# Kernel optimization log

Hardware: AMD Instinct MI355X
Metric: run time of the kernel (lower is better)

The kernel has to match this reference:

```python
import jax, jax.numpy as jnp
import numpy as np

N = 262144  # nodes
E = 262144  # edges (child -> parent)
X = 128     # x_size
H = 128     # h_size


def setup_inputs() -> dict:
    key = jax.random.key(0)
    ks = jax.random.split(key, 10)
    s = 1.0 / np.sqrt(H)
    return {
        "token_embeds": jax.random.normal(ks[0], (N, X), jnp.float32),
        "h": jax.random.normal(ks[1], (N, H), jnp.float32),
        "c": jax.random.normal(ks[2], (N, H), jnp.float32),
        "src": jax.random.randint(ks[3], (E,), 0, N),
        "dst": jax.random.randint(ks[4], (E,), 0, N),
        "W_iou": jax.random.normal(ks[5], (3 * H, X), jnp.float32) * s,
        "U_iou": jax.random.normal(ks[6], (3 * H, H), jnp.float32) * s,
        "b_iou": jnp.zeros((1, 3 * H), jnp.float32),
        "U_f_w": jax.random.normal(ks[7], (H, H), jnp.float32) * s,
        "U_f_b": jnp.zeros((H,), jnp.float32),
        "W_f_w": jax.random.normal(ks[8], (H, X), jnp.float32) * s,
        "b_f": jnp.zeros((1, H), jnp.float32),
    }


def reference(token_embeds, h, c, src, dst, W_iou, U_iou, b_iou, U_f_w, U_f_b, W_f_w, b_f):
    # message + reduce: gather children's h/c and sum into parent mailboxes
    h_sum = jax.ops.segment_sum(h[src], dst, num_segments=N)  # [N,H]
    c_sum = jax.ops.segment_sum(c[src], dst, num_segments=N)  # [N,H]
    # forget gate is per-node, so sum_k f*c_k == f * sum_k c_k
    f = jax.nn.sigmoid(token_embeds @ W_f_w.T + h @ U_f_w.T + U_f_b + b_f)  # [N,H]
    c_red = f * c_sum
    iou = token_embeds @ W_iou.T + h_sum @ U_iou.T + b_iou  # [N,3H]
    i, o, u = jnp.split(iou, 3, axis=1)
    c_new = jax.nn.sigmoid(i) * jnp.tanh(u) + c_red
    h_new = jax.nn.sigmoid(o) * jnp.tanh(c_new)
    return h_new, c_new
```

## Files before the change

### kernel.cpp

```cpp
#include <hip/hip_runtime.h>
#include <hip/hip_bf16.h>
#include <cstdint>

#define HH 128
#define XX 128

typedef __attribute__((ext_vector_type(8))) short short8;
typedef __attribute__((ext_vector_type(4))) short short4_;
typedef __attribute__((ext_vector_type(4))) float float4_;
typedef __attribute__((ext_vector_type(8))) _Float16 half8_;

__device__ __forceinline__ float sigmoidf_(float x) {
  return 1.f / (1.f + __expf(-x));
}
__device__ __forceinline__ float tanhf_(float x) {
  float e = __expf(-2.f * fabsf(x));
  float t = (1.f - e) / (1.f + e);
  return copysignf(t, x);
}

__global__ __launch_bounds__(256) void hist_kernel(const int* __restrict__ dst,
                                                   int* __restrict__ cnt, int E) {
  int e = blockIdx.x * 256 + threadIdx.x;
  if (e < E) atomicAdd(&cnt[dst[e]], 1);
}

__global__ __launch_bounds__(256) void scan_block_sum(const int* __restrict__ cnt,
                                                      int* __restrict__ bsum) {
  __shared__ int red[256];
  int b = blockIdx.x, t = threadIdx.x;
  int base = b * 1024 + t * 4;
  int s = cnt[base] + cnt[base + 1] + cnt[base + 2] + cnt[base + 3];
  red[t] = s;
  __syncthreads();
  for (int off = 128; off > 0; off >>= 1) {
    if (t < off) red[t] += red[t + off];
    __syncthreads();
  }
  if (t == 0) bsum[b] = red[0];
}

__global__ __launch_bounds__(256) void scan_top(const int* __restrict__ bsum,
                                                int* __restrict__ boff,
                                                int* __restrict__ row_ptr, int N,
                                                int E) {
  __shared__ int tmp[256];
  int t = threadIdx.x;
  int own = bsum[t];
  tmp[t] = own;
  __syncthreads();
  for (int off = 1; off < 256; off <<= 1) {
    int x = (t >= off) ? tmp[t - off] : 0;
    __syncthreads();
    tmp[t] += x;
    __syncthreads();
  }
  boff[t] = tmp[t] - own;
  if (t == 0) row_ptr[N] = E;
}

__global__ __launch_bounds__(256) void scan_fill(const int* __restrict__ cnt,
                                                 const int* __restrict__ boff,
                                                 int* __restrict__ row_ptr,
                                                 int* __restrict__ row_fill) {
  __shared__ int tsum[256];
  int b = blockIdx.x, t = threadIdx.x;
  int base = b * 1024 + t * 4;
  int v0 = cnt[base], v1 = cnt[base + 1], v2 = cnt[base + 2], v3 = cnt[base + 3];
  int s = v0 + v1 + v2 + v3;
  tsum[t] = s;
  __syncthreads();
  for (int off = 1; off < 256; off <<= 1) {
    int x = (t >= off) ? tsum[t - off] : 0;
    __syncthreads();
    tsum[t] += x;
    __syncthreads();
  }
  int excl = tsum[t] - s + boff[b];
  int p0 = excl, p1 = p0 + v0, p2 = p1 + v1, p3 = p2 + v2;
  row_ptr[base] = p0;
  row_ptr[base + 1] = p1;
  row_ptr[base + 2] = p2;
  row_ptr[base + 3] = p3;
  row_fill[base] = p0;
  row_fill[base + 1] = p1;
  row_fill[base + 2] = p2;
  row_fill[base + 3] = p3;
}

__global__ __launch_bounds__(256) void fill_kernel(const int* __restrict__ src,
                                                   const int* __restrict__ dst,
                                                   int* __restrict__ row_fill,
                                                   int* __restrict__ edge_src,
                                                   int E) {
  int e = blockIdx.x * 256 + threadIdx.x;
  if (e >= E) return;
  int pos = atomicAdd(&row_fill[dst[e]], 1);
  edge_src[pos] = src[e];
}

__global__ __launch_bounds__(256) void prep_kernel(
    const float* __restrict__ W_iou, const float* __restrict__ U_iou,
    const float* __restrict__ b_iou, const float* __restrict__ U_f_w,
    const float* __restrict__ U_f_b, const float* __restrict__ W_f_w,
    const float* __restrict__ b_f, unsigned short* __restrict__ Bh,
    float* __restrict__ bias) {
  int tid = blockIdx.x * 256 + threadIdx.x;
  int kg = tid & 3;
  int c16 = (tid >> 2) & 15;
  int ks = (tid >> 6) & 7;
  int w = (tid >> 9) & 7;
  int g = (tid >> 12) & 3;
  int col = w * 16 + c16;
  int kbase = ks * 32 + kg * 8;
#pragma unroll
  for (int j = 0; j < 8; ++j) {
    int k = kbase + j;
    float v;
    if (g < 3) {
      v = (k < 128) ? W_iou[(size_t)(g * 128 + col) * 128 + k]
                    : U_iou[(size_t)(g * 128 + col) * 128 + (k - 128)];
    } else {
      v = (k < 128) ? W_f_w[(size_t)col * 128 + k]
                    : U_f_w[(size_t)col * 128 + (k - 128)];
    }
    Bh[(size_t)tid * 8 + j] = __builtin_bit_cast(unsigned short, (_Float16)v);
  }
  if (tid < 512) {
    int gg = tid >> 7, cc = tid & 127;
    bias[tid] = (gg < 3) ? b_iou[gg * 128 + cc] : (U_f_b[cc] + b_f[cc]);
  }
}


__device__ __forceinline__ void stage_f16(unsigned short* su, int a, int node,
                                          int k4, float4_ v) {
  unsigned short hq[4];
#pragma unroll
  for (int j = 0; j < 4; ++j)
    hq[j] = __builtin_bit_cast(unsigned short, (_Float16)v[j]);
  int off = k4 ^ ((node & 7) << 3);
  *reinterpret_cast<short4_*>(&su[a * 4096 + node * 128 + off]) =
      *reinterpret_cast<const short4_*>(hq);
}

__device__ __forceinline__ half8_ read_frag(const unsigned short* su, int a,
                                            int node, int kbase, int lane) {
  int k = kbase + ((lane >> 4) << 3);
  int off = k ^ ((node & 7) << 3);
  short8 s = *reinterpret_cast<const short8*>(&su[a * 4096 + node * 128 + off]);
  return __builtin_bit_cast(half8_, s);
}

__device__ __forceinline__ int cw(int row, int col) {
  return row * 128 + (col ^ ((row & 7) << 2));
}

__global__ __launch_bounds__(512, 6) void fused_mfma_kernel(
    const float* __restrict__ te, const float* __restrict__ h,
    const float* __restrict__ c, const int* __restrict__ row_ptr,
    const int* __restrict__ edge_src, const unsigned short* __restrict__ Bh,
    const float* __restrict__ bias, float* __restrict__ out_h,
    float* __restrict__ out_c) {
  __shared__ float4_ smem4[2048];
  unsigned short* su = (unsigned short*)smem4;

  const int t = threadIdx.x;
  const int node0 = blockIdx.x * 32;

  const int nl = t >> 4;
  const int sub = t & 15;
  const int e0 = row_ptr[node0 + nl];
  const int e1 = row_ptr[node0 + nl + 1];
  int s0 = (e0 < e1) ? edge_src[e0] : 0;
  float4_ ph[2], pc[2];
  if (e0 < e1) {
    const float* hp = h + (size_t)s0 * HH + sub * 8;
    const float* cp = c + (size_t)s0 * HH + sub * 8;
#pragma unroll
    for (int i = 0; i < 2; ++i) {
      ph[i] = *reinterpret_cast<const float4_*>(hp + i * 4);
      pc[i] = *reinterpret_cast<const float4_*>(cp + i * 4);
    }
  }

#pragma unroll
  for (int i = 0; i < 2; ++i) {
    int q = t + i * 512;
    int node = q >> 5;
    int k4 = (q & 31) * 4;
    float4_ v =
        *reinterpret_cast<const float4_*>(te + (size_t)(node0 + node) * XX + k4);
    stage_f16(su, 0, node, k4, v);
    v = *reinterpret_cast<const float4_*>(h + (size_t)(node0 + node) * HH + k4);
    stage_f16(su, 2, node, k4, v);
  }

  {
    float hs[8], cs[8];
#pragma unroll
    for (int j = 0; j < 8; ++j) {
      hs[j] = 0.f;
      cs[j] = 0.f;
    }
    if (e0 < e1) {
#pragma unroll
      for (int i = 0; i < 2; ++i)
#pragma unroll
        for (int j = 0; j < 4; ++j) {
          hs[i * 4 + j] += ph[i][j];
          cs[i * 4 + j] += pc[i][j];
        }
    }
    for (int e = e0 + 1; e < e1; ++e) {
      int s = edge_src[e];
      const float* hp = h + (size_t)s * HH + sub * 8;
      const float* cp = c + (size_t)s * HH + sub * 8;
#pragma unroll
      for (int i = 0; i < 2; ++i) {
        float4_ hv = *reinterpret_cast<const float4_*>(hp + i * 4);
        float4_ cv = *reinterpret_cast<const float4_*>(cp + i * 4);
#pragma unroll
        for (int j = 0; j < 4; ++j) {
          hs[i * 4 + j] += hv[j];
          cs[i * 4 + j] += cv[j];
        }
      }
    }
#pragma unroll
    for (int i = 0; i < 2; ++i) {
      float4_ v = {hs[i * 4], hs[i * 4 + 1], hs[i * 4 + 2], hs[i * 4 + 3]};
      stage_f16(su, 1, nl, sub * 8 + i * 4, v);
      float4_ cv = {cs[i * 4], cs[i * 4 + 1], cs[i * 4 + 2], cs[i * 4 + 3]};
      stage_f16(su, 3, nl, sub * 8 + i * 4, cv);
    }
  }
  __syncthreads();

  const int lane = t & 63;
  const int wave = t >> 6;
  const int wc = wave * 16;
  const int cl = lane & 15;
  const int kq = lane >> 4;

  float4_ acc[4][2];
#pragma unroll
  for (int g = 0; g < 4; ++g)
#pragma unroll
    for (int m = 0; m < 2; ++m) acc[g][m] = (float4_){0.f, 0.f, 0.f, 0.f};

  for (int ks = 0; ks < 8; ++ks) {
    half8_ bh[4];
#pragma unroll
    for (int g = 0; g < 4; ++g) {
      size_t boff = (size_t)(((g * 8 + wave) * 8 + ks) * 512) + cl * 32 + kq * 8;
      bh[g] = __builtin_bit_cast(half8_,
                                 *reinterpret_cast<const short8*>(&Bh[boff]));
    }
    if (ks < 4) {
      int kbase = ks * 32;
#pragma unroll
      for (int m = 0; m < 2; ++m) {
        half8_ ah = read_frag(su, 0, m * 16 + cl, kbase, lane);
#pragma unroll
        for (int g = 0; g < 4; ++g)
          acc[g][m] = __builtin_amdgcn_mfma_f32_16x16x32_f16(ah, bh[g],
                                                             acc[g][m], 0, 0, 0);
      }
    } else {
      int kbase = (ks - 4) * 32;
#pragma unroll
      for (int m = 0; m < 2; ++m) {
        half8_ ah = read_frag(su, 1, m * 16 + cl, kbase, lane);
        half8_ fh = read_frag(su, 2, m * 16 + cl, kbase, lane);
#pragma unroll
        for (int g = 0; g < 3; ++g)
          acc[g][m] = __builtin_amdgcn_mfma_f32_16x16x32_f16(ah, bh[g],
                                                             acc[g][m], 0, 0, 0);
        acc[3][m] = __builtin_amdgcn_mfma_f32_16x16x32_f16(fh, bh[3],
                                                           acc[3][m], 0, 0, 0);
      }
    }
  }

  const int col = wc + cl;
  float bi = bias[0 * 128 + col];
  float bo = bias[1 * 128 + col];
  float bu = bias[2 * 128 + col];
  float bf = bias[3 * 128 + col];
  float csv[2][4];
#pragma unroll
  for (int m = 0; m < 2; ++m)
#pragma unroll
    for (int r = 0; r < 4; ++r) {
      int row = m * 16 + kq * 4 + r;
      unsigned short hb = su[3 * 4096 + row * 128 + (col ^ ((row & 7) << 3))];
      csv[m][r] = (float)__builtin_bit_cast(_Float16, hb);
    }

  __syncthreads();

  float* oh = (float*)smem4;
  float* oc = (float*)smem4 + 4096;

#pragma unroll
  for (int m = 0; m < 2; ++m)
#pragma unroll
    for (int r = 0; r < 4; ++r) {
      int rowl = m * 16 + kq * 4 + r;
      float ig = sigmoidf_(acc[0][m][r] + bi);
      float og = sigmoidf_(acc[1][m][r] + bo);
      float ug = tanhf_(acc[2][m][r] + bu);
      float fg = sigmoidf_(acc[3][m][r] + bf);
      float cn = fmaf(ig, ug, fg * csv[m][r]);
      int wadr = cw(rowl, col);
      oc[wadr] = cn;
      oh[wadr] = og * tanhf_(cn);
    }
  __syncthreads();

#pragma unroll
  for (int i = 0; i < 2; ++i) {
    int q = t + i * 512;
    int rr = q >> 5;
    int k4 = (q & 31) * 4;
    int wadr = rr * 128 + (k4 ^ ((rr & 7) << 2));
    *reinterpret_cast<float4_*>(out_h + (size_t)(node0 + rr) * HH + k4) =
        *reinterpret_cast<const float4_*>(&oh[wadr]);
    *reinterpret_cast<float4_*>(out_c + (size_t)(node0 + rr) * HH + k4) =
        *reinterpret_cast<const float4_*>(&oc[wadr]);
  }
}

extern "C" void kernel_launch(void* const* d_in, const int* in_sizes, int n_in,
                              void* d_out, int out_size, void* d_ws, size_t ws_size,
                              hipStream_t stream) {
  const float* te = (const float*)d_in[0];
  const float* h = (const float*)d_in[1];
  const float* c = (const float*)d_in[2];
  const int* src = (const int*)d_in[3];
  const int* dst = (const int*)d_in[4];
  const float* W_iou = (const float*)d_in[5];
  const float* U_iou = (const float*)d_in[6];
  const float* b_iou = (const float*)d_in[7];
  const float* U_f_w = (const float*)d_in[8];
  const float* U_f_b = (const float*)d_in[9];
  const float* W_f_w = (const float*)d_in[10];
  const float* b_f = (const float*)d_in[11];

  const int N = in_sizes[1] / HH;
  const int E = in_sizes[3];

  float* out_h = (float*)d_out;
  float* out_c = out_h + (size_t)N * HH;

  char* ws = (char*)d_ws;
  unsigned short* Bh = (unsigned short*)ws;
  float* bias = (float*)(Bh + 4 * 8 * 8 * 16 * 4 * 8);
  int* cnt = (int*)(bias + 512);
  int* row_ptr = cnt + N;
  int* row_fill = row_ptr + N + 4;
  int* edge_src = row_fill + N;
  int* bsum = edge_src + E;
  int* boff = bsum + 256;

  hipMemsetAsync(cnt, 0, (size_t)N * sizeof(int), stream);

  hist_kernel<<<(E + 255) / 256, 256, 0, stream>>>(dst, cnt, E);
  scan_block_sum<<<N / 1024, 256, 0, stream>>>(cnt, bsum);
  scan_top<<<1, 256, 0, stream>>>(bsum, boff, row_ptr, N, E);
  scan_fill<<<N / 1024, 256, 0, stream>>>(cnt, boff, row_ptr, row_fill);
  fill_kernel<<<(E + 255) / 256, 256, 0, stream>>>(src, dst, row_fill, edge_src, E);

  prep_kernel<<<64, 256, 0, stream>>>(W_iou, U_iou, b_iou, U_f_w, U_f_b, W_f_w,
                                      b_f, Bh, bias);

  fused_mfma_kernel<<<N / 32, 512, 0, stream>>>(te, h, c, row_ptr, edge_src, Bh,
                                                bias, out_h, out_c);
}
```

Baseline: 321.9 us.

## Split child gather into separate kernel and double fused tile to 64 nodes

Moves the child h/c segment-sum out of the MFMA kernel into a dedicated gather kernel. That kernel writes packed fp16 sums, pre-swizzled, into the out_h buffer, which serves as scratch. The fused kernel then copies these sums straight into LDS, handles 64 nodes per block with twice the LDS and accumulators, and uses packed cvt_pkrtz conversions. The aim is to take the irregular gather latency off the MFMA kernel and raise B-fragment reuse. The cost is an extra round trip of the sum buffer through global memory and lower occupancy in the fused kernel.

```diff
diff --git a/kernel.cpp b/kernel.cpp
--- a/kernel.cpp
+++ b/kernel.cpp
@@ -9,6 +9,9 @@
 typedef __attribute__((ext_vector_type(4))) short short4_;
 typedef __attribute__((ext_vector_type(4))) float float4_;
 typedef __attribute__((ext_vector_type(8))) _Float16 half8_;
+typedef __attribute__((ext_vector_type(2))) _Float16 half2_;
+typedef __attribute__((ext_vector_type(2))) unsigned int uint2_;
+typedef __attribute__((ext_vector_type(4))) unsigned int uint4_;
 
 __device__ __forceinline__ float sigmoidf_(float x) {
   return 1.f / (1.f + __expf(-x));
@@ -132,23 +135,76 @@
   }
 }
 
-
-__device__ __forceinline__ void stage_f16(unsigned short* su, int a, int node,
-                                          int k4, float4_ v) {
-  unsigned short hq[4];
-#pragma unroll
-  for (int j = 0; j < 4; ++j)
-    hq[j] = __builtin_bit_cast(unsigned short, (_Float16)v[j]);
+__global__ __launch_bounds__(256, 8) void gather_kernel(
+    const float* __restrict__ h, const float* __restrict__ c,
+    const int* __restrict__ row_ptr, const int* __restrict__ edge_src,
+    float* __restrict__ sums) {
+  const int gt = blockIdx.x * 256 + threadIdx.x;
+  const int wid = gt >> 6;
+  const int lane = gt & 63;
+  const int node = (wid << 2) + (lane >> 4);
+  const int sub = lane & 15;
+
+  const int e0 = row_ptr[node];
+  const int e1 = row_ptr[node + 1];
+
+  float hs[8] = {0.f, 0.f, 0.f, 0.f, 0.f, 0.f, 0.f, 0.f};
+  float cs[8] = {0.f, 0.f, 0.f, 0.f, 0.f, 0.f, 0.f, 0.f};
+
+  for (int e = e0; e < e1; ++e) {
+    int s = edge_src[e];
+    const float* hp = h + (size_t)s * HH + sub * 8;
+    const float* cp = c + (size_t)s * HH + sub * 8;
+    float4_ h0 = *reinterpret_cast<const float4_*>(hp);
+    float4_ h1 = *reinterpret_cast<const float4_*>(hp + 4);
+    float4_ c0 = *reinterpret_cast<const float4_*>(cp);
+    float4_ c1 = *reinterpret_cast<const float4_*>(cp + 4);
+#pragma unroll
+    for (int j = 0; j < 4; ++j) {
+      hs[j] += h0[j];
+      hs[4 + j] += h1[j];
+      cs[j] += c0[j];
+      cs[4 + j] += c1[j];
+    }
+  }
+
+  uint4_ hv, cv;
+#pragma unroll
+  for (int i = 0; i < 4; ++i) {
+    hv[i] = __builtin_bit_cast(unsigned int,
+                               __builtin_amdgcn_cvt_pkrtz(hs[2 * i], hs[2 * i + 1]));
+    cv[i] = __builtin_bit_cast(unsigned int,
+                               __builtin_amdgcn_cvt_pkrtz(cs[2 * i], cs[2 * i + 1]));
+  }
+  int off = (sub * 8) ^ ((node & 7) << 3);
+  char* row = (char*)sums + (size_t)node * 512;
+  *reinterpret_cast<uint4_*>(row + off * 2) = hv;
+  *reinterpret_cast<uint4_*>(row + 256 + off * 2) = cv;
+}
+
+__device__ __forceinline__ void stage_pk(unsigned short* su, int baseH, int node,
+                                         int k4, float4_ v) {
+  unsigned int u0 = __builtin_bit_cast(unsigned int,
+                                       __builtin_amdgcn_cvt_pkrtz(v[0], v[1]));
+  unsigned int u1 = __builtin_bit_cast(unsigned int,
+                                       __builtin_amdgcn_cvt_pkrtz(v[2], v[3]));
   int off = k4 ^ ((node & 7) << 3);
-  *reinterpret_cast<short4_*>(&su[a * 4096 + node * 128 + off]) =
-      *reinterpret_cast<const short4_*>(hq);
-}
-
-__device__ __forceinline__ half8_ read_frag(const unsigned short* su, int a,
-                                            int node, int kbase, int lane) {
+  *reinterpret_cast<uint2_*>(&su[baseH + node * 128 + off]) = (uint2_){u0, u1};
+}
+
+__device__ __forceinline__ half8_ read_frag128(const unsigned short* su, int baseH,
+                                               int node, int kbase, int lane) {
   int k = kbase + ((lane >> 4) << 3);
   int off = k ^ ((node & 7) << 3);
-  short8 s = *reinterpret_cast<const short8*>(&su[a * 4096 + node * 128 + off]);
+  short8 s = *reinterpret_cast<const short8*>(&su[baseH + node * 128 + off]);
+  return __builtin_bit_cast(half8_, s);
+}
+
+__device__ __forceinline__ half8_ read_fragS(const unsigned short* su, int node,
+                                             int kbase, int lane) {
+  int k = kbase + ((lane >> 4) << 3);
+  int off = k ^ ((node & 7) << 3);
+  short8 s = *reinterpret_cast<const short8*>(&su[16384 + node * 256 + off]);
   return __builtin_bit_cast(half8_, s);
 }
 
@@ -156,84 +212,37 @@
   return row * 128 + (col ^ ((row & 7) << 2));
 }
 
-__global__ __launch_bounds__(512, 6) void fused_mfma_kernel(
+__global__ __launch_bounds__(512, 4) void fused_mfma_kernel(
     const float* __restrict__ te, const float* __restrict__ h,
-    const float* __restrict__ c, const int* __restrict__ row_ptr,
-    const int* __restrict__ edge_src, const unsigned short* __restrict__ Bh,
+    const float* __restrict__ sums, const unsigned short* __restrict__ Bh,
     const float* __restrict__ bias, float* __restrict__ out_h,
     float* __restrict__ out_c) {
-  __shared__ float4_ smem4[2048];
+  __shared__ float4_ smem4[4096];
   unsigned short* su = (unsigned short*)smem4;
 
   const int t = threadIdx.x;
-  const int node0 = blockIdx.x * 32;
-
-  const int nl = t >> 4;
-  const int sub = t & 15;
-  const int e0 = row_ptr[node0 + nl];
-  const int e1 = row_ptr[node0 + nl + 1];
-  int s0 = (e0 < e1) ? edge_src[e0] : 0;
-  float4_ ph[2], pc[2];
-  if (e0 < e1) {
-    const float* hp = h + (size_t)s0 * HH + sub * 8;
-    const float* cp = c + (size_t)s0 * HH + sub * 8;
-#pragma unroll
-    for (int i = 0; i < 2; ++i) {
-      ph[i] = *reinterpret_cast<const float4_*>(hp + i * 4);
-      pc[i] = *reinterpret_cast<const float4_*>(cp + i * 4);
-    }
-  }
-
-#pragma unroll
-  for (int i = 0; i < 2; ++i) {
+  const int node0 = blockIdx.x * 64;
+
+  {
+    const char* sbase = (const char*)sums + (size_t)node0 * 512;
+    char* dbase = (char*)smem4 + 32768;
+#pragma unroll
+    for (int i = 0; i < 4; ++i) {
+      int q = t + i * 512;
+      *reinterpret_cast<uint4_*>(dbase + q * 16) =
+          *reinterpret_cast<const uint4_*>(sbase + q * 16);
+    }
+  }
+#pragma unroll
+  for (int i = 0; i < 4; ++i) {
     int q = t + i * 512;
     int node = q >> 5;
     int k4 = (q & 31) * 4;
     float4_ v =
         *reinterpret_cast<const float4_*>(te + (size_t)(node0 + node) * XX + k4);
-    stage_f16(su, 0, node, k4, v);
+    stage_pk(su, 0, node, k4, v);
     v = *reinterpret_cast<const float4_*>(h + (size_t)(node0 + node) * HH + k4);
-    stage_f16(su, 2, node, k4, v);
-  }
-
-  {
-    float hs[8], cs[8];
-#pragma unroll
-    for (int j = 0; j < 8; ++j) {
-      hs[j] = 0.f;
-      cs[j] = 0.f;
-    }
-    if (e0 < e1) {
-#pragma unroll
-      for (int i = 0; i < 2; ++i)
-#pragma unroll
-        for (int j = 0; j < 4; ++j) {
-          hs[i * 4 + j] += ph[i][j];
-          cs[i * 4 + j] += pc[i][j];
-        }
-    }
-    for (int e = e0 + 1; e < e1; ++e) {
-      int s = edge_src[e];
-      const float* hp = h + (size_t)s * HH + sub * 8;
-      const float* cp = c + (size_t)s * HH + sub * 8;
-#pragma unroll
-      for (int i = 0; i < 2; ++i) {
-        float4_ hv = *reinterpret_cast<const float4_*>(hp + i * 4);
-        float4_ cv = *reinterpret_cast<const float4_*>(cp + i * 4);
-#pragma unroll
-        for (int j = 0; j < 4; ++j) {
-          hs[i * 4 + j] += hv[j];
-          cs[i * 4 + j] += cv[j];
-        }
-      }
-    }
-#pragma unroll
-    for (int i = 0; i < 2; ++i) {
-      float4_ v = {hs[i * 4], hs[i * 4 + 1], hs[i * 4 + 2], hs[i * 4 + 3]};
-      stage_f16(su, 1, nl, sub * 8 + i * 4, v);
-      float4_ cv = {cs[i * 4], cs[i * 4 + 1], cs[i * 4 + 2], cs[i * 4 + 3]};
-      stage_f16(su, 3, nl, sub * 8 + i * 4, cv);
-    }
+    stage_pk(su, 8192, node, k4, v);
   }
   __syncthreads();
 
@@ -243,11 +252,11 @@
   const int cl = lane & 15;
   const int kq = lane >> 4;
 
-  float4_ acc[4][2];
+  float4_ acc[4][4];
 #pragma unroll
   for (int g = 0; g < 4; ++g)
 #pragma unroll
-    for (int m = 0; m < 2; ++m) acc[g][m] = (float4_){0.f, 0.f, 0.f, 0.f};
+    for (int m = 0; m < 4; ++m) acc[g][m] = (float4_){0.f, 0.f, 0.f, 0.f};
 
   for (int ks = 0; ks < 8; ++ks) {
     half8_ bh[4];
@@ -260,8 +269,8 @@
     if (ks < 4) {
       int kbase = ks * 32;
 #pragma unroll
-      for (int m = 0; m < 2; ++m) {
-        half8_ ah = read_frag(su, 0, m * 16 + cl, kbase, lane);
+      for (int m = 0; m < 4; ++m) {
+        half8_ ah = read_frag128(su, 0, m * 16 + cl, kbase, lane);
 #pragma unroll
         for (int g = 0; g < 4; ++g)
           acc[g][m] = __builtin_amdgcn_mfma_f32_16x16x32_f16(ah, bh[g],
@@ -270,9 +279,9 @@
     } else {
       int kbase = (ks - 4) * 32;
 #pragma unroll
-      for (int m = 0; m < 2; ++m) {
-        half8_ ah = read_frag(su, 1, m * 16 + cl, kbase, lane);
-        half8_ fh = read_frag(su, 2, m * 16 + cl, kbase, lane);
+      for (int m = 0; m < 4; ++m) {
+        half8_ ah = read_fragS(su, m * 16 + cl, kbase, lane);
+        half8_ fh = read_frag128(su, 8192, m * 16 + cl, kbase, lane);
 #pragma unroll
         for (int g = 0; g < 3; ++g)
           acc[g][m] = __builtin_amdgcn_mfma_f32_16x16x32_f16(ah, bh[g],
@@ -288,23 +297,24 @@
   float bo = bias[1 * 128 + col];
   float bu = bias[2 * 128 + col];
   float bf = bias[3 * 128 + col];
-  float csv[2][4];
-#pragma unroll
-  for (int m = 0; m < 2; ++m)
+  float csv[4][4];
+#pragma unroll
+  for (int m = 0; m < 4; ++m)
 #pragma unroll
     for (int r = 0; r < 4; ++r) {
       int row = m * 16 + kq * 4 + r;
-      unsigned short hb = su[3 * 4096 + row * 128 + (col ^ ((row & 7) << 3))];
+      unsigned short hb =
+          su[16384 + row * 256 + 128 + (col ^ ((row & 7) << 3))];
       csv[m][r] = (float)__builtin_bit_cast(_Float16, hb);
     }
 
   __syncthreads();
 
   float* oh = (float*)smem4;
-  float* oc = (float*)smem4 + 4096;
-
-#pragma unroll
-  for (int m = 0; m < 2; ++m)
+  float* oc = (float*)smem4 + 8192;
+
+#pragma unroll
+  for (int m = 0; m < 4; ++m)
 #pragma unroll
     for (int r = 0; r < 4; ++r) {
       int rowl = m * 16 + kq * 4 + r;
@@ -320,7 +330,7 @@
   __syncthreads();
 
 #pragma unroll
-  for (int i = 0; i < 2; ++i) {
+  for (int i = 0; i < 4; ++i) {
     int q = t + i * 512;
     int rr = q >> 5;
     int k4 = (q & 31) * 4;
@@ -375,6 +385,8 @@
   prep_kernel<<<64, 256, 0, stream>>>(W_iou, U_iou, b_iou, U_f_w, U_f_b, W_f_w,
                                       b_f, Bh, bias);
 
-  fused_mfma_kernel<<<N / 32, 512, 0, stream>>>(te, h, c, row_ptr, edge_src, Bh,
-                                                bias, out_h, out_c);
-}
+  gather_kernel<<<N / 16, 256, 0, stream>>>(h, c, row_ptr, edge_src, out_h);
+
+  fused_mfma_kernel<<<N / 64, 512, 0, stream>>>(te, h, out_h, Bh, bias, out_h,
+                                                out_c);
+}
```

Measured after the change: 342.3 us. 6.3% more time.

## Make fused kernel persistent with double-buffered tiles overlapping loads and MFMA

Applied to the files above, without the earlier changes.

The fused kernel becomes persistent: 512 blocks each loop over 16 tiles of 32 nodes. The next tile's row_ptr, token embedding and h loads are issued before the current tile's MFMA compute, and the staged fp16 operands go into a second LDS buffer so memory latency overlaps compute. Conversion now uses packed cvt_pkrtz, and bias loads are hoisted out of the loop. LDS doubles to 64KB and the occupancy hint drops from 6 to 4, which lowers parallelism and latency hiding across blocks. The gather loop for children is still serialized inside finishC after compute.

```diff
diff --git a/kernel.cpp b/kernel.cpp
--- a/kernel.cpp
+++ b/kernel.cpp
@@ -9,6 +9,8 @@
 typedef __attribute__((ext_vector_type(4))) short short4_;
 typedef __attribute__((ext_vector_type(4))) float float4_;
 typedef __attribute__((ext_vector_type(8))) _Float16 half8_;
+typedef __attribute__((ext_vector_type(2))) unsigned int uint2_;
+typedef __attribute__((ext_vector_type(4))) unsigned int uint4_;
 
 __device__ __forceinline__ float sigmoidf_(float x) {
   return 1.f / (1.f + __expf(-x));
@@ -133,22 +135,11 @@
 }
 
 
-__device__ __forceinline__ void stage_f16(unsigned short* su, int a, int node,
-                                          int k4, float4_ v) {
-  unsigned short hq[4];
-#pragma unroll
-  for (int j = 0; j < 4; ++j)
-    hq[j] = __builtin_bit_cast(unsigned short, (_Float16)v[j]);
-  int off = k4 ^ ((node & 7) << 3);
-  *reinterpret_cast<short4_*>(&su[a * 4096 + node * 128 + off]) =
-      *reinterpret_cast<const short4_*>(hq);
-}
-
-__device__ __forceinline__ half8_ read_frag(const unsigned short* su, int a,
+__device__ __forceinline__ half8_ read_frag(const unsigned short* su, int baseH,
                                             int node, int kbase, int lane) {
   int k = kbase + ((lane >> 4) << 3);
   int off = k ^ ((node & 7) << 3);
-  short8 s = *reinterpret_cast<const short8*>(&su[a * 4096 + node * 128 + off]);
+  short8 s = *reinterpret_cast<const short8*>(&su[baseH + node * 128 + off]);
   return __builtin_bit_cast(half8_, s);
 }
 
@@ -156,179 +147,195 @@
   return row * 128 + (col ^ ((row & 7) << 2));
 }
 
-__global__ __launch_bounds__(512, 6) void fused_mfma_kernel(
+__device__ __forceinline__ uint4_ pack8(const float* v) {
+  uint4_ r;
+#pragma unroll
+  for (int i = 0; i < 4; ++i)
+    r[i] = __builtin_bit_cast(unsigned int,
+                              __builtin_amdgcn_cvt_pkrtz(v[2 * i], v[2 * i + 1]));
+  return r;
+}
+
+__global__ __launch_bounds__(512, 4) void fused_mfma_kernel(
     const float* __restrict__ te, const float* __restrict__ h,
     const float* __restrict__ c, const int* __restrict__ row_ptr,
     const int* __restrict__ edge_src, const unsigned short* __restrict__ Bh,
     const float* __restrict__ bias, float* __restrict__ out_h,
-    float* __restrict__ out_c) {
-  __shared__ float4_ smem4[2048];
+    float* __restrict__ out_c, int tpb) {
+  __shared__ float4_ smem4[4096];
   unsigned short* su = (unsigned short*)smem4;
 
   const int t = threadIdx.x;
-  const int node0 = blockIdx.x * 32;
-
+  const int lane = t & 63;
+  const int wave = t >> 6;
   const int nl = t >> 4;
   const int sub = t & 15;
-  const int e0 = row_ptr[node0 + nl];
-  const int e1 = row_ptr[node0 + nl + 1];
-  int s0 = (e0 < e1) ? edge_src[e0] : 0;
-  float4_ ph[2], pc[2];
-  if (e0 < e1) {
-    const float* hp = h + (size_t)s0 * HH + sub * 8;
-    const float* cp = c + (size_t)s0 * HH + sub * 8;
-#pragma unroll
-    for (int i = 0; i < 2; ++i) {
-      ph[i] = *reinterpret_cast<const float4_*>(hp + i * 4);
-      pc[i] = *reinterpret_cast<const float4_*>(cp + i * 4);
-    }
-  }
-
-#pragma unroll
-  for (int i = 0; i < 2; ++i) {
-    int q = t + i * 512;
-    int node = q >> 5;
-    int k4 = (q & 31) * 4;
-    float4_ v =
-        *reinterpret_cast<const float4_*>(te + (size_t)(node0 + node) * XX + k4);
-    stage_f16(su, 0, node, k4, v);
-    v = *reinterpret_cast<const float4_*>(h + (size_t)(node0 + node) * HH + k4);
-    stage_f16(su, 2, node, k4, v);
-  }
-
-  {
-    float hs[8], cs[8];
-#pragma unroll
-    for (int j = 0; j < 8; ++j) {
-      hs[j] = 0.f;
-      cs[j] = 0.f;
-    }
-    if (e0 < e1) {
-#pragma unroll
-      for (int i = 0; i < 2; ++i)
-#pragma unroll
-        for (int j = 0; j < 4; ++j) {
-          hs[i * 4 + j] += ph[i][j];
-          cs[i * 4 + j] += pc[i][j];
-        }
-    }
-    for (int e = e0 + 1; e < e1; ++e) {
-      int s = edge_src[e];
-      const float* hp = h + (size_t)s * HH + sub * 8;
-      const float* cp = c + (size_t)s * HH + sub * 8;
-#pragma unroll
-      for (int i = 0; i < 2; ++i) {
-        float4_ hv = *reinterpret_cast<const float4_*>(hp + i * 4);
-        float4_ cv = *reinterpret_cast<const float4_*>(cp + i * 4);
-#pragma unroll
-        for (int j = 0; j < 4; ++j) {
-          hs[i * 4 + j] += hv[j];
-          cs[i * 4 + j] += cv[j];
-        }
-      }
-    }
-#pragma unroll
-    for (int i = 0; i < 2; ++i) {
-      float4_ v = {hs[i * 4], hs[i * 4 + 1], hs[i * 4 + 2], hs[i * 4 + 3]};
-      stage_f16(su, 1, nl, sub * 8 + i * 4, v);
-      float4_ cv = {cs[i * 4], cs[i * 4 + 1], cs[i * 4 + 2], cs[i * 4 + 3]};
-      stage_f16(su, 3, nl, sub * 8 + i * 4, cv);
-    }
-  }
-  __syncthreads();
-
-  const int lane = t & 63;
-  const int wave = t >> 6;
   const int wc = wave * 16;
   const int cl = lane & 15;
   const int kq = lane >> 4;
-
-  float4_ acc[4][2];
-#pragma unroll
-  for (int g = 0; g < 4; ++g)
-#pragma unroll
-    for (int m = 0; m < 2; ++m) acc[g][m] = (float4_){0.f, 0.f, 0.f, 0.f};
-
-  for (int ks = 0; ks < 8; ++ks) {
-    half8_ bh[4];
-#pragma unroll
-    for (int g = 0; g < 4; ++g) {
-      size_t boff = (size_t)(((g * 8 + wave) * 8 + ks) * 512) + cl * 32 + kq * 8;
-      bh[g] = __builtin_bit_cast(half8_,
-                                 *reinterpret_cast<const short8*>(&Bh[boff]));
+  const int col = wc + cl;
+
+  const float bi = bias[col];
+  const float bo = bias[128 + col];
+  const float bu = bias[256 + col];
+  const float bf = bias[384 + col];
+
+  const int tile0 = blockIdx.x * tpb;
+
+  float4_ pt0, pt1, ph0, ph1;
+  int e0 = 0, e1 = 0, shead = 0;
+
+  auto issueA = [&](int tile) {
+    int node = tile * 32 + nl;
+    e0 = row_ptr[node];
+    e1 = row_ptr[node + 1];
+    const float* tp = te + (size_t)node * XX + sub * 8;
+    const float* hp = h + (size_t)node * HH + sub * 8;
+    pt0 = *reinterpret_cast<const float4_*>(tp);
+    pt1 = *reinterpret_cast<const float4_*>(tp + 4);
+    ph0 = *reinterpret_cast<const float4_*>(hp);
+    ph1 = *reinterpret_cast<const float4_*>(hp + 4);
+    shead = edge_src[(e0 < e1) ? e0 : 0];
+  };
+
+  auto finishC = [&](int bb) {
+    float hs[8] = {0.f, 0.f, 0.f, 0.f, 0.f, 0.f, 0.f, 0.f};
+    float cs[8] = {0.f, 0.f, 0.f, 0.f, 0.f, 0.f, 0.f, 0.f};
+    if (e0 < e1) {
+      const float* hp = h + (size_t)shead * HH + sub * 8;
+      const float* cp = c + (size_t)shead * HH + sub * 8;
+      float4_ h0 = *reinterpret_cast<const float4_*>(hp);
+      float4_ h1 = *reinterpret_cast<const float4_*>(hp + 4);
+      float4_ c0 = *reinterpret_cast<const float4_*>(cp);
+      float4_ c1 = *reinterpret_cast<const float4_*>(cp + 4);
+#pragma unroll
+      for (int j = 0; j < 4; ++j) {
+        hs[j] += h0[j];
+        hs[4 + j] += h1[j];
+        cs[j] += c0[j];
+        cs[4 + j] += c1[j];
+      }
+      for (int e = e0 + 1; e < e1; ++e) {
+        int s = edge_src[e];
+        const float* hp2 = h + (size_t)s * HH + sub * 8;
+        const float* cp2 = c + (size_t)s * HH + sub * 8;
+        float4_ a0 = *reinterpret_cast<const float4_*>(hp2);
+        float4_ a1 = *reinterpret_cast<const float4_*>(hp2 + 4);
+        float4_ b0 = *reinterpret_cast<const float4_*>(cp2);
+        float4_ b1 = *reinterpret_cast<const float4_*>(cp2 + 4);
+#pragma unroll
+        for (int j = 0; j < 4; ++j) {
+          hs[j] += a0[j];
+          hs[4 + j] += a1[j];
+          cs[j] += b0[j];
+          cs[4 + j] += b1[j];
+        }
+      }
     }
-    if (ks < 4) {
-      int kbase = ks * 32;
-#pragma unroll
-      for (int m = 0; m < 2; ++m) {
-        half8_ ah = read_frag(su, 0, m * 16 + cl, kbase, lane);
-#pragma unroll
-        for (int g = 0; g < 4; ++g)
-          acc[g][m] = __builtin_amdgcn_mfma_f32_16x16x32_f16(ah, bh[g],
-                                                             acc[g][m], 0, 0, 0);
-      }
-    } else {
-      int kbase = (ks - 4) * 32;
-#pragma unroll
-      for (int m = 0; m < 2; ++m) {
-        half8_ ah = read_frag(su, 1, m * 16 + cl, kbase, lane);
-        half8_ fh = read_frag(su, 2, m * 16 + cl, kbase, lane);
-#pragma unroll
-        for (int g = 0; g < 3; ++g)
-          acc[g][m] = __builtin_amdgcn_mfma_f32_16x16x32_f16(ah, bh[g],
-                                                             acc[g][m], 0, 0, 0);
-        acc[3][m] = __builtin_amdgcn_mfma_f32_16x16x32_f16(fh, bh[3],
-                                                           acc[3][m], 0, 0, 0);
+    int off = (sub * 8) ^ ((nl & 7) << 3);
+    float tv[8] = {pt0[0], pt0[1], pt0[2], pt0[3], pt1[0], pt1[1], pt1[2], pt1[3]};
+    float hv[8] = {ph0[0], ph0[1], ph0[2], ph0[3], ph1[0], ph1[1], ph1[2], ph1[3]};
+    *reinterpret_cast<uint4_*>(&su[bb + nl * 128 + off]) = pack8(tv);
+    *reinterpret_cast<uint4_*>(&su[bb + 4096 + nl * 128 + off]) = pack8(hv);
+    *reinterpret_cast<uint4_*>(&su[bb + 8192 + nl * 128 + off]) = pack8(hs);
+    *reinterpret_cast<uint4_*>(&su[bb + 12288 + nl * 128 + off]) = pack8(cs);
+  };
+
+  auto computeB = [&](int tile, int bb) {
+    float4_ acc[4][2];
+#pragma unroll
+    for (int g = 0; g < 4; ++g)
+#pragma unroll
+      for (int m = 0; m < 2; ++m) acc[g][m] = (float4_){0.f, 0.f, 0.f, 0.f};
+
+    for (int ks = 0; ks < 8; ++ks) {
+      half8_ bh[4];
+#pragma unroll
+      for (int g = 0; g < 4; ++g) {
+        size_t boff = (size_t)(((g * 8 + wave) * 8 + ks) * 512) + cl * 32 + kq * 8;
+        bh[g] = __builtin_bit_cast(half8_,
+                                   *reinterpret_cast<const short8*>(&Bh[boff]));
+      }
+      if (ks < 4) {
+        int kbase = ks * 32;
+#pragma unroll
+        for (int m = 0; m < 2; ++m) {
+          half8_ ah = read_frag(su, bb, m * 16 + cl, kbase, lane);
+#pragma unroll
+          for (int g = 0; g < 4; ++g)
+            acc[g][m] = __builtin_amdgcn_mfma_f32_16x16x32_f16(ah, bh[g],
+                                                               acc[g][m], 0, 0, 0);
+        }
+      } else {
+        int kbase = (ks - 4) * 32;
+#pragma unroll
+        for (int m = 0; m < 2; ++m) {
+          half8_ ah = read_frag(su, bb + 8192, m * 16 + cl, kbase, lane);
+          half8_ fh = read_frag(su, bb + 4096, m * 16 + cl, kbase, lane);
+#pragma unroll
+          for (int g = 0; g < 3; ++g)
+            acc[g][m] = __builtin_amdgcn_mfma_f32_16x16x32_f16(ah, bh[g],
+                                                               acc[g][m], 0, 0, 0);
+          acc[3][m] = __builtin_amdgcn_mfma_f32_16x16x32_f16(fh, bh[3],
+                                                             acc[3][m], 0, 0, 0);
+        }
       }
     }
-  }
-
-  const int col = wc + cl;
-  float bi = bias[0 * 128 + col];
-  float bo = bias[1 * 128 + col];
-  float bu = bias[2 * 128 + col];
-  float bf = bias[3 * 128 + col];
-  float csv[2][4];
-#pragma unroll
-  for (int m = 0; m < 2; ++m)
-#pragma unroll
-    for (int r = 0; r < 4; ++r) {
-      int row = m * 16 + kq * 4 + r;
-      unsigned short hb = su[3 * 4096 + row * 128 + (col ^ ((row & 7) << 3))];
-      csv[m][r] = (float)__builtin_bit_cast(_Float16, hb);
+
+    float csv[2][4];
+#pragma unroll
+    for (int m = 0; m < 2; ++m)
+#pragma unroll
+      for (int r = 0; r < 4; ++r) {
+        int row = m * 16 + kq * 4 + r;
+        unsigned short hb = su[bb + 12288 + row * 128 + (col ^ ((row & 7) << 3))];
+        csv[m][r] = (float)__builtin_bit_cast(_Float16, hb);
+      }
+    __syncthreads();
+
+    float* ow = (float*)smem4 + (bb >> 1);
+#pragma unroll
+    for (int m = 0; m < 2; ++m)
+#pragma unroll
+      for (int r = 0; r < 4; ++r) {
+        int rowl = m * 16 + kq * 4 + r;
+        float ig = sigmoidf_(acc[0][m][r] + bi);
+        float og = sigmoidf_(acc[1][m][r] + bo);
+        float ug = tanhf_(acc[2][m][r] + bu);
+        float fg = sigmoidf_(acc[3][m][r] + bf);
+        float cn = fmaf(ig, ug, fg * csv[m][r]);
+        int wadr = cw(rowl, col);
+        ow[wadr] = og * tanhf_(cn);
+        ow[4096 + wadr] = cn;
+      }
+    __syncthreads();
+
+    int node0 = tile * 32;
+#pragma unroll
+    for (int i = 0; i < 2; ++i) {
+      int q = t + i * 512;
+      int rr = q >> 5;
+      int k4 = (q & 31) * 4;
+      int wadr = rr * 128 + (k4 ^ ((rr & 7) << 2));
+      *reinterpret_cast<float4_*>(out_h + (size_t)(node0 + rr) * HH + k4) =
+          *reinterpret_cast<const float4_*>(&ow[wadr]);
+      *reinterpret_cast<float4_*>(out_c + (size_t)(node0 + rr) * HH + k4) =
+          *reinterpret_cast<const float4_*>(&ow[4096 + wadr]);
     }
-
+  };
+
+  issueA(tile0);
+  finishC(0);
   __syncthreads();
 
-  float* oh = (float*)smem4;
-  float* oc = (float*)smem4 + 4096;
-
-#pragma unroll
-  for (int m = 0; m < 2; ++m)
-#pragma unroll
-    for (int r = 0; r < 4; ++r) {
-      int rowl = m * 16 + kq * 4 + r;
-      float ig = sigmoidf_(acc[0][m][r] + bi);
-      float og = sigmoidf_(acc[1][m][r] + bo);
-      float ug = tanhf_(acc[2][m][r] + bu);
-      float fg = sigmoidf_(acc[3][m][r] + bf);
-      float cn = fmaf(ig, ug, fg * csv[m][r]);
-      int wadr = cw(rowl, col);
-      oc[wadr] = cn;
-      oh[wadr] = og * tanhf_(cn);
-    }
-  __syncthreads();
-
-#pragma unroll
-  for (int i = 0; i < 2; ++i) {
-    int q = t + i * 512;
-    int rr = q >> 5;
-    int k4 = (q & 31) * 4;
-    int wadr = rr * 128 + (k4 ^ ((rr & 7) << 2));
-    *reinterpret_cast<float4_*>(out_h + (size_t)(node0 + rr) * HH + k4) =
-        *reinterpret_cast<const float4_*>(&oh[wadr]);
-    *reinterpret_cast<float4_*>(out_c + (size_t)(node0 + rr) * HH + k4) =
-        *reinterpret_cast<const float4_*>(&oc[wadr]);
+  int cur = 0;
+  for (int i = 0; i < tpb; ++i) {
+    bool have = (i + 1) < tpb;
+    if (have) issueA(tile0 + i + 1);
+    computeB(tile0 + i, cur ? 16384 : 0);
+    if (have) finishC(cur ? 0 : 16384);
+    __syncthreads();
+    cur ^= 1;
   }
 }
 
@@ -375,6 +382,8 @@
   prep_kernel<<<64, 256, 0, stream>>>(W_iou, U_iou, b_iou, U_f_w, U_f_b, W_f_w,
                                       b_f, Bh, bias);
 
-  fused_mfma_kernel<<<N / 32, 512, 0, stream>>>(te, h, c, row_ptr, edge_src, Bh,
-                                                bias, out_h, out_c);
-}
+  const int nblocks = 512;
+  const int tpb = (N / 32) / nblocks;
+  fused_mfma_kernel<<<nblocks, 512, 0, stream>>>(te, h, c, row_ptr, edge_src,
+                                                 Bh, bias, out_h, out_c, tpb);
+}
```

New measurement: 632.8 us. +96.6%, slower.
